# Kernel tuning notes

Hardware: AMD Instinct MI355X
Metric: run time of the kernel (lower is better)

## Reference

```python
import jax, jax.numpy as jnp
import numpy as np

H = 1024

def setup_inputs() -> dict:
    key = jax.random.key(0)
    ks = jax.random.split(key, 7)
    s = 1.0 / np.sqrt(H)
    return {
        "hidden_states": jax.random.normal(ks[0], (4, 2048, H), dtype=jnp.float32),
        "Wq": jax.random.uniform(ks[1], (H, H), jnp.float32, -s, s),
        "bq": jax.random.uniform(ks[2], (H,), jnp.float32, -s, s),
        "Wk": jax.random.uniform(ks[3], (H, H), jnp.float32, -s, s),
        "bk": jax.random.uniform(ks[4], (H,), jnp.float32, -s, s),
        "Wv": jax.random.uniform(ks[5], (H, H), jnp.float32, -s, s),
        "bv": jax.random.uniform(ks[6], (H,), jnp.float32, -s, s),
    }

def reference(hidden_states, Wq, bq, Wk, bk, Wv, bv):
    # Linear projections (torch Linear: x @ W.T + b)
    q = hidden_states @ Wq.T + bq  # [B,S,H]
    k = hidden_states @ Wk.T + bk
    v = hidden_states @ Wv.T + bv
    # Unscaled attention
    probs = jax.nn.softmax(jnp.einsum("bqh,bkh->bqk", q, k), axis=-1)  # [B,S,S]
    attention_scores = jnp.sum(probs, axis=-2)  # [B,S] column sums
    context = jnp.einsum("bqk,bkh->bqh", probs, v)  # [B,S,H]
    return (context, attention_scores)
```

## Files before the change

kernel.cpp:

```cpp
#include <hip/hip_runtime.h>
#include <stdint.h>


typedef __attribute__((ext_vector_type(8))) short short8;
typedef __attribute__((ext_vector_type(4))) float floatx4;
typedef __attribute__((ext_vector_type(4))) unsigned short ushort4v;
typedef unsigned short u16;

__device__ __forceinline__ u16 f2bf(float f) {
  union { float f; uint32_t u; } v; v.f = f;
  uint32_t u = v.u;
  return (u16)((u + 0x7FFFu + ((u >> 16) & 1u)) >> 16);
}
__device__ __forceinline__ float bf2f(u16 h) {
  union { uint32_t u; float f; } v; v.u = ((uint32_t)h) << 16; return v.f;
}

#define AS3(p) ((__attribute__((address_space(3))) void*)(uint32_t)(uintptr_t)(p))
#define AS1(p) ((__attribute__((address_space(1))) void*)(uintptr_t)(p))

__global__ __launch_bounds__(256) void cvt_all_kernel(
    const float* __restrict__ hs, const float* __restrict__ Wq,
    const float* __restrict__ Wk, const float* __restrict__ Wv,
    u16* __restrict__ hsb, u16* __restrict__ Wb, float* __restrict__ lsum) {
  const int bx = blockIdx.x;
  const float* src;
  u16* dst;
  int i;
  if (bx < 8192) {
    i = bx * 1024 + threadIdx.x * 4;
    src = hs; dst = hsb;
  } else {
    const int idx = bx - 8192;
    const int p = idx >> 10, blk = idx & 1023;
    src = (p == 0) ? Wq : (p == 1) ? Wk : Wv;
    dst = Wb + p * 1048576;
    i = blk * 1024 + threadIdx.x * 4;
  }
  const float4 v = *(const float4*)(src + i);
  ushort4v o;
  o[0] = f2bf(v.x); o[1] = f2bf(v.y); o[2] = f2bf(v.z); o[3] = f2bf(v.w);
  *(ushort4v*)(dst + i) = o;
  if (bx == 0) {
    float4 z = {0.f, 0.f, 0.f, 0.f};
#pragma unroll
    for (int k = 0; k < 8; ++k)
      *(float4*)(lsum + threadIdx.x * 32 + k * 4) = z;
  }
}

#define DC_SLOT 24576

template <int NT>
__device__ __forceinline__ void deep_core(const u16* __restrict__ A,
                                          const u16* __restrict__ B,
                                          int lda, int ldb,
                                          u16* smem, floatx4 acc[4][4]) {
  const int tid  = threadIdx.x;
  const int lane = tid & 63;
  const int w    = tid >> 6;
  const int wm   = w >> 1;
  const int wn   = w & 1;
  const int fr   = lane & 15;
  const int quad = lane >> 4;
  const int pc0  = (quad ^ (fr & 7)) * 8;
  const int pc1  = ((4 + quad) ^ (fr & 7)) * 8;

  const u16* pA[4]; uint32_t dA[4];
#pragma unroll
  for (int j = 0; j < 4; ++j) {
    const int c = tid + j * 512, row = c >> 3, kc = c & 7;
    pA[j] = A + row * lda + (kc ^ (row & 7)) * 8;
    dA[j] = c * 8;
  }
  const u16* pB[2]; uint32_t dB[2];
#pragma unroll
  for (int j = 0; j < 2; ++j) {
    const int c = tid + j * 512, row = c >> 3, kc = c & 7;
    pB[j] = B + row * ldb + (kc ^ (row & 7)) * 8;
    dB[j] = 16384 + c * 8;
  }

#define DC_STA(u) do { u16* s_ = smem + ((u) % 3) * DC_SLOT;                                  \
    _Pragma("unroll") for (int j_ = 0; j_ < 4; ++j_)                                           \
      __builtin_amdgcn_global_load_lds(AS1(pA[j_] + (u) * 64), AS3(s_ + dA[j_]), 16, 0, 0);   \
  } while (0)
#define DC_STB(u) do { u16* s_ = smem + ((u) % 3) * DC_SLOT;                                  \
    _Pragma("unroll") for (int j_ = 0; j_ < 2; ++j_)                                           \
      __builtin_amdgcn_global_load_lds(AS1(pB[j_] + (u) * 64), AS3(s_ + dB[j_]), 16, 0, 0);   \
  } while (0)

  DC_STA(0); DC_STB(0); DC_STA(1); DC_STB(1);
  asm volatile("s_waitcnt vmcnt(6)" ::: "memory");
  __builtin_amdgcn_s_barrier();

  const int arow0 = wm * 64 + fr;
  const int brow0 = wn * 64 + fr;

#pragma unroll
  for (int t = 0; t < NT; ++t) {
    const u16* sA = smem + (t % 3) * DC_SLOT;
    const u16* sB = sA + 16384;
    short8 af[4], bf[4];

#pragma unroll
    for (int mi = 0; mi < 4; ++mi)
      af[mi] = *(const short8*)(sA + (arow0 + mi * 16) * 64 + pc0);
#pragma unroll
    for (int ni = 0; ni < 4; ++ni)
      bf[ni] = *(const short8*)(sB + (brow0 + ni * 16) * 64 + pc0);
    if (t < NT - 2) DC_STA(t + 2);
    __builtin_amdgcn_s_barrier();
    asm volatile("s_waitcnt lgkmcnt(0)" ::: "memory");
    __builtin_amdgcn_sched_barrier(0);
    __builtin_amdgcn_s_setprio(1);
#pragma unroll
    for (int mi = 0; mi < 4; ++mi)
#pragma unroll
      for (int ni = 0; ni < 4; ++ni)
        acc[mi][ni] = __builtin_amdgcn_mfma_f32_16x16x32_bf16(af[mi], bf[ni],
                                                              acc[mi][ni], 0, 0, 0);
    __builtin_amdgcn_s_setprio(0);
    __builtin_amdgcn_s_barrier();

#pragma unroll
    for (int mi = 0; mi < 4; ++mi)
      af[mi] = *(const short8*)(sA + (arow0 + mi * 16) * 64 + pc1);
#pragma unroll
    for (int ni = 0; ni < 4; ++ni)
      bf[ni] = *(const short8*)(sB + (brow0 + ni * 16) * 64 + pc1);
    if (t < NT - 2) {
      DC_STB(t + 2);
      asm volatile("s_waitcnt vmcnt(6)" ::: "memory");
    } else {
      asm volatile("s_waitcnt vmcnt(0)" ::: "memory");
    }
    __builtin_amdgcn_s_barrier();
    asm volatile("s_waitcnt lgkmcnt(0)" ::: "memory");
    __builtin_amdgcn_sched_barrier(0);
    __builtin_amdgcn_s_setprio(1);
#pragma unroll
    for (int mi = 0; mi < 4; ++mi)
#pragma unroll
      for (int ni = 0; ni < 4; ++ni)
        acc[mi][ni] = __builtin_amdgcn_mfma_f32_16x16x32_bf16(af[mi], bf[ni],
                                                              acc[mi][ni], 0, 0, 0);
    __builtin_amdgcn_s_setprio(0);
    __builtin_amdgcn_s_barrier();
  }
#undef DC_STA
#undef DC_STB
}

__global__ __launch_bounds__(512, 2) void proj_deep_kernel(
    const u16* __restrict__ hsb, const u16* __restrict__ Wb,
    const float* __restrict__ bq, const float* __restrict__ bk,
    const float* __restrict__ bv,
    u16* __restrict__ qo, u16* __restrict__ ko, u16* __restrict__ vt) {
  extern __shared__ __align__(16) u16 smem[];
  floatx4 acc[4][4];
#pragma unroll
  for (int i = 0; i < 4; ++i)
#pragma unroll
    for (int j = 0; j < 4; ++j) acc[i][j] = {0.f, 0.f, 0.f, 0.f};

  const int p    = blockIdx.z;
  const int flat = blockIdx.x + blockIdx.y * 8;
  const int swz  = (flat & 7) * 32 + (flat >> 3);
  const int m0   = (swz >> 3) * 256;
  const int n0   = (swz & 7) * 128;

  deep_core<16>(hsb + m0 * 1024, Wb + p * 1048576 + n0 * 1024, 1024, 1024, smem, acc);

  const float* bias = (p == 0) ? bq : (p == 1) ? bk : bv;
  const int lane = threadIdx.x & 63, w = threadIdx.x >> 6;
  const int wm = w >> 1, wn = w & 1;
  const int fr = lane & 15, rg4 = (lane >> 4) * 4;

  if (p < 2) {
    u16* out = (p == 0) ? qo : ko;
#pragma unroll
    for (int mi = 0; mi < 4; ++mi)
#pragma unroll
      for (int ni = 0; ni < 4; ++ni) {
        const int n = n0 + wn * 64 + ni * 16 + fr;
        const float bn = bias[n];
#pragma unroll
        for (int r = 0; r < 4; ++r) {
          const int m = m0 + wm * 64 + mi * 16 + rg4 + r;
          out[m * 1024 + n] = f2bf(acc[mi][ni][r] + bn);
        }
      }
  } else {
#pragma unroll
    for (int mi = 0; mi < 4; ++mi) {
      const int mbase = m0 + wm * 64 + mi * 16 + rg4;
      const int b = mbase >> 11, s = mbase & 2047;
#pragma unroll
      for (int ni = 0; ni < 4; ++ni) {
        const int n = n0 + wn * 64 + ni * 16 + fr;
        const float bn = bias[n];
        ushort4v pk;
#pragma unroll
        for (int r = 0; r < 4; ++r) pk[r] = f2bf(acc[mi][ni][r] + bn);
        *(ushort4v*)(vt + b * 2097152 + n * 2048 + s) = pk;
      }
    }
  }
}

__global__ __launch_bounds__(512, 2) void logits_deep_kernel(
    const u16* __restrict__ q, const u16* __restrict__ k,
    u16* __restrict__ E, float* __restrict__ lsum) {
  extern __shared__ __align__(16) u16 smem[];
  floatx4 acc[4][4];
#pragma unroll
  for (int i = 0; i < 4; ++i)
#pragma unroll
    for (int j = 0; j < 4; ++j) acc[i][j] = {0.f, 0.f, 0.f, 0.f};

  const int flat = blockIdx.x + blockIdx.y * 16 + blockIdx.z * 128;
  const int swz  = (flat & 7) * 64 + (flat >> 3);
  const int b    = swz >> 7;
  const int m0   = ((swz >> 4) & 7) * 256;
  const int n0   = (swz & 15) * 128;

  deep_core<16>(q + (b * 2048 + m0) * 1024, k + (b * 2048 + n0) * 1024,
                1024, 1024, smem, acc);

  const int lane = threadIdx.x & 63, w = threadIdx.x >> 6;
  const int wm = w >> 1, wn = w & 1;
  const int fr = lane & 15, quad = lane >> 4;
  u16* Eb = E + b * 4194304;
  float* lb = lsum + b * 2048;

#pragma unroll
  for (int mi = 0; mi < 4; ++mi) {
    floatx4 rs = {0.f, 0.f, 0.f, 0.f};
    const int rbase = m0 + wm * 64 + mi * 16 + quad * 4;
#pragma unroll
    for (int ni = 0; ni < 4; ++ni) {
      const int n = n0 + wn * 64 + ni * 16 + fr;
#pragma unroll
      for (int r = 0; r < 4; ++r) {
        const float e = __expf(acc[mi][ni][r]);
        rs[r] += e;
        Eb[(rbase + r) * 2048 + n] = f2bf(e);
      }
    }
#pragma unroll
    for (int off = 1; off < 16; off <<= 1) {
      rs[0] += __shfl_xor(rs[0], off, 64);
      rs[1] += __shfl_xor(rs[1], off, 64);
      rs[2] += __shfl_xor(rs[2], off, 64);
      rs[3] += __shfl_xor(rs[3], off, 64);
    }
    if (fr == 0) {
#pragma unroll
      for (int r = 0; r < 4; ++r) atomicAdd(&lb[rbase + r], rs[r]);
    }
  }
}

__global__ __launch_bounds__(512, 2) void context_deep_kernel(
    const u16* __restrict__ E, const u16* __restrict__ vt,
    const float* __restrict__ lsum, float* __restrict__ out) {
  extern __shared__ __align__(16) u16 smem[];
  floatx4 acc[4][4];
#pragma unroll
  for (int i = 0; i < 4; ++i)
#pragma unroll
    for (int j = 0; j < 4; ++j) acc[i][j] = {0.f, 0.f, 0.f, 0.f};

  const int flat = blockIdx.x + blockIdx.y * 8 + blockIdx.z * 64;
  const int swz  = (flat & 7) * 32 + (flat >> 3);
  const int b    = swz >> 6;
  const int m0   = ((swz >> 3) & 7) * 256;
  const int n0   = (swz & 7) * 128;

  deep_core<32>(E + b * 4194304 + m0 * 2048, vt + b * 2097152 + n0 * 2048,
                2048, 2048, smem, acc);

  const int lane = threadIdx.x & 63, w = threadIdx.x >> 6;
  const int wm = w >> 1, wn = w & 1;
  const int fr = lane & 15, rg4 = (lane >> 4) * 4;
  const float* lb = lsum + b * 2048;

#pragma unroll
  for (int mi = 0; mi < 4; ++mi) {
    const int rbase = m0 + wm * 64 + mi * 16 + rg4;
    float rinv[4];
#pragma unroll
    for (int r = 0; r < 4; ++r) rinv[r] = 1.0f / lb[rbase + r];
#pragma unroll
    for (int ni = 0; ni < 4; ++ni) {
      const int n = n0 + wn * 64 + ni * 16 + fr;
#pragma unroll
      for (int r = 0; r < 4; ++r)
        out[(b * 2048 + rbase + r) * 1024 + n] = acc[mi][ni][r] * rinv[r];
    }
  }
}

__global__ __launch_bounds__(256) void colsum_part_kernel(
    const u16* __restrict__ E, const float* __restrict__ lsum,
    float* __restrict__ part) {
  const int b  = blockIdx.x;
  const int g  = blockIdx.y;
  const int q0 = g * 64;
  const int j  = threadIdx.x * 8;
  const u16* Eb = E + b * 4194304;
  const float* lb = lsum + b * 2048;
  float acc[8];
#pragma unroll
  for (int c = 0; c < 8; ++c) acc[c] = 0.f;
  for (int r = 0; r < 64; ++r) {
    const int qi = q0 + r;
    const float rinv = 1.0f / lb[qi];
    const short8 ev = *(const short8*)(Eb + qi * 2048 + j);
#pragma unroll
    for (int c = 0; c < 8; ++c) acc[c] += bf2f((u16)ev[c]) * rinv;
  }
  float* pb = part + (b * 32 + g) * 2048 + j;
#pragma unroll
  for (int c = 0; c < 8; ++c) pb[c] = acc[c];
}

__global__ __launch_bounds__(256) void colsum_reduce_kernel(
    const float* __restrict__ part, float* __restrict__ scores) {
  const int b = blockIdx.x;
  const int j = blockIdx.y * 256 + threadIdx.x;
  const float* pb = part + b * 32 * 2048 + j;
  float s = 0.f;
#pragma unroll
  for (int g = 0; g < 32; ++g) s += pb[g * 2048];
  scores[b * 2048 + j] = s;
}

extern "C" void kernel_launch(void* const* d_in, const int* in_sizes, int n_in,
                              void* d_out, int out_size, void* d_ws, size_t ws_size,
                              hipStream_t stream) {
  const float* hs = (const float*)d_in[0];
  const float* Wq = (const float*)d_in[1];
  const float* bq = (const float*)d_in[2];
  const float* Wk = (const float*)d_in[3];
  const float* bk = (const float*)d_in[4];
  const float* Wv = (const float*)d_in[5];
  const float* bv = (const float*)d_in[6];

  char* ws = (char*)d_ws;
  u16*   qw  = (u16*)(ws);
  u16*   kw  = (u16*)(ws + (16u << 20));
  u16*   vtw = (u16*)(ws + (32u << 20));
  float* lw  = (float*)(ws + (48u << 20));
  float* pw  = (float*)(ws + (48u << 20) + (128u << 10));
  u16*   hsb = (u16*)(ws + (49u << 20));
  u16*   Wb  = (u16*)(ws + (65u << 20));
  u16*   Ew  = (u16*)(ws + (49u << 20));

  float* outc = (float*)d_out;
  float* outs = outc + 8388608;

  static int s_attr_done = 0;
  if (!s_attr_done) {
    (void)hipFuncSetAttribute((const void*)proj_deep_kernel,
                              hipFuncAttributeMaxDynamicSharedMemorySize, 147456);
    (void)hipFuncSetAttribute((const void*)logits_deep_kernel,
                              hipFuncAttributeMaxDynamicSharedMemorySize, 147456);
    (void)hipFuncSetAttribute((const void*)context_deep_kernel,
                              hipFuncAttributeMaxDynamicSharedMemorySize, 147456);
    s_attr_done = 1;
  }

  cvt_all_kernel<<<11264, 256, 0, stream>>>(hs, Wq, Wk, Wv, hsb, Wb, lw);
  proj_deep_kernel<<<dim3(8, 32, 3), 512, 147456, stream>>>(hsb, Wb, bq, bk, bv, qw, kw, vtw);
  logits_deep_kernel<<<dim3(16, 8, 4), 512, 147456, stream>>>(qw, kw, Ew, lw);
  context_deep_kernel<<<dim3(8, 8, 4), 512, 147456, stream>>>(Ew, vtw, lw, outc);
  colsum_part_kernel<<<dim3(4, 32), 256, 0, stream>>>(Ew, lw, pw);
  colsum_reduce_kernel<<<dim3(4, 8), 256, 0, stream>>>(pw, outs);
}
```

Before: 241.4 us.

## Use 256x256 logits tiles with quadrant-pipelined MFMA and widen conversion and colsum work

Replaces the 256x128 logits GEMM with a 256x256-tile kernel. It double-buffers LDS and splits each k-step into four quadrant MFMA phases, interleaved with global-to-LDS loads for the next step, which raises operand reuse and halves the block count. The fp32-to-bf16 conversion kernel now handles 8 elements per thread, and the colsum partial kernel gets twice the blocks with 4 columns each for more parallelism. It also adjusts the deep_core tail wait. The risks are higher register pressure and fewer blocks (256) on the large logits GEMM, with possible occupancy or tail effects.

```diff
diff --git a/kernel.cpp b/kernel.cpp
--- a/kernel.cpp
+++ b/kernel.cpp
@@ -5,6 +5,7 @@
 typedef __attribute__((ext_vector_type(8))) short short8;
 typedef __attribute__((ext_vector_type(4))) float floatx4;
 typedef __attribute__((ext_vector_type(4))) unsigned short ushort4v;
+typedef __attribute__((ext_vector_type(8))) unsigned short ushort8v;
 typedef unsigned short u16;
 
 __device__ __forceinline__ u16 f2bf(float f) {
@@ -27,20 +28,22 @@
   const float* src;
   u16* dst;
   int i;
-  if (bx < 8192) {
-    i = bx * 1024 + threadIdx.x * 4;
+  if (bx < 4096) {
+    i = bx * 2048 + threadIdx.x * 8;
     src = hs; dst = hsb;
   } else {
-    const int idx = bx - 8192;
-    const int p = idx >> 10, blk = idx & 1023;
+    const int idx = bx - 4096;
+    const int p = idx >> 9, blk = idx & 511;
     src = (p == 0) ? Wq : (p == 1) ? Wk : Wv;
     dst = Wb + p * 1048576;
-    i = blk * 1024 + threadIdx.x * 4;
-  }
-  const float4 v = *(const float4*)(src + i);
-  ushort4v o;
-  o[0] = f2bf(v.x); o[1] = f2bf(v.y); o[2] = f2bf(v.z); o[3] = f2bf(v.w);
-  *(ushort4v*)(dst + i) = o;
+    i = blk * 2048 + threadIdx.x * 8;
+  }
+  const float4 v0 = *(const float4*)(src + i);
+  const float4 v1 = *(const float4*)(src + i + 4);
+  ushort8v o;
+  o[0] = f2bf(v0.x); o[1] = f2bf(v0.y); o[2] = f2bf(v0.z); o[3] = f2bf(v0.w);
+  o[4] = f2bf(v1.x); o[5] = f2bf(v1.y); o[6] = f2bf(v1.z); o[7] = f2bf(v1.w);
+  *(ushort8v*)(dst + i) = o;
   if (bx == 0) {
     float4 z = {0.f, 0.f, 0.f, 0.f};
 #pragma unroll
@@ -49,7 +52,7 @@
   }
 }
 
-#define DC_SLOT 24576
+#define DC_SLOTU 24576
 
 template <int NT>
 __device__ __forceinline__ void deep_core(const u16* __restrict__ A,
@@ -81,11 +84,11 @@
     dB[j] = 16384 + c * 8;
   }
 
-#define DC_STA(u) do { u16* s_ = smem + ((u) % 3) * DC_SLOT;                                  \
+#define DC_STA(u) do { u16* s_ = smem + ((u) % 3) * DC_SLOTU;                                  \
     _Pragma("unroll") for (int j_ = 0; j_ < 4; ++j_)                                           \
       __builtin_amdgcn_global_load_lds(AS1(pA[j_] + (u) * 64), AS3(s_ + dA[j_]), 16, 0, 0);   \
   } while (0)
-#define DC_STB(u) do { u16* s_ = smem + ((u) % 3) * DC_SLOT;                                  \
+#define DC_STB(u) do { u16* s_ = smem + ((u) % 3) * DC_SLOTU;                                  \
     _Pragma("unroll") for (int j_ = 0; j_ < 2; ++j_)                                           \
       __builtin_amdgcn_global_load_lds(AS1(pB[j_] + (u) * 64), AS3(s_ + dB[j_]), 16, 0, 0);   \
   } while (0)
@@ -99,7 +102,7 @@
 
 #pragma unroll
   for (int t = 0; t < NT; ++t) {
-    const u16* sA = smem + (t % 3) * DC_SLOT;
+    const u16* sA = smem + (t % 3) * DC_SLOTU;
     const u16* sB = sA + 16384;
     short8 af[4], bf[4];
 
@@ -132,7 +135,7 @@
     if (t < NT - 2) {
       DC_STB(t + 2);
       asm volatile("s_waitcnt vmcnt(6)" ::: "memory");
-    } else {
+    } else if (t == NT - 2) {
       asm volatile("s_waitcnt vmcnt(0)" ::: "memory");
     }
     __builtin_amdgcn_s_barrier();
@@ -209,57 +212,157 @@
   }
 }
 
-__global__ __launch_bounds__(512, 2) void logits_deep_kernel(
+__global__ __launch_bounds__(512, 2) void logits_q4_kernel(
     const u16* __restrict__ q, const u16* __restrict__ k,
     u16* __restrict__ E, float* __restrict__ lsum) {
   extern __shared__ __align__(16) u16 smem[];
-  floatx4 acc[4][4];
-#pragma unroll
-  for (int i = 0; i < 4; ++i)
-#pragma unroll
-    for (int j = 0; j < 4; ++j) acc[i][j] = {0.f, 0.f, 0.f, 0.f};
-
-  const int flat = blockIdx.x + blockIdx.y * 16 + blockIdx.z * 128;
-  const int swz  = (flat & 7) * 64 + (flat >> 3);
-  const int b    = swz >> 7;
-  const int m0   = ((swz >> 4) & 7) * 256;
-  const int n0   = (swz & 15) * 128;
-
-  deep_core<16>(q + (b * 2048 + m0) * 1024, k + (b * 2048 + n0) * 1024,
-                1024, 1024, smem, acc);
-
-  const int lane = threadIdx.x & 63, w = threadIdx.x >> 6;
-  const int wm = w >> 1, wn = w & 1;
-  const int fr = lane & 15, quad = lane >> 4;
+  const int tid  = threadIdx.x;
+  const int lane = tid & 63;
+  const int w    = tid >> 6;
+  const int wr4  = w >> 2;
+  const int wc4  = w & 3;
+  const int fr   = lane & 15;
+  const int kq   = lane >> 4;
+  const int pc0  = (kq ^ (fr & 7)) * 8;
+  const int pc1  = ((4 + kq) ^ (fr & 7)) * 8;
+
+  const int flat = blockIdx.x + blockIdx.y * 8 + blockIdx.z * 64;
+  const int swz  = (flat & 7) * 32 + (flat >> 3);
+  const int b    = swz >> 6;
+  const int m0   = ((swz >> 3) & 7) * 256;
+  const int n0   = (swz & 7) * 256;
+
+  const u16* Ag = q + (b * 2048 + m0) * 1024;
+  const u16* Bg = k + (b * 2048 + n0) * 1024;
+
+  const u16* pAs[2]; const u16* pBs[2]; uint32_t dof[2];
+#pragma unroll
+  for (int j = 0; j < 2; ++j) {
+    const int c = tid + j * 512, rl = c >> 3, kc = c & 7;
+    const int gc = (kc ^ (rl & 7)) * 8;
+    pAs[j] = Ag + rl * 1024 + gc;
+    pBs[j] = Bg + rl * 1024 + gc;
+    dof[j] = c * 8;
+  }
+#define ST_A(h, tt, sbase) do { _Pragma("unroll") for (int j_ = 0; j_ < 2; ++j_)      \
+    __builtin_amdgcn_global_load_lds(AS1(pAs[j_] + (h) * 131072 + (tt) * 64),         \
+        AS3(smem + (sbase) + (h) * 8192 + dof[j_]), 16, 0, 0); } while (0)
+#define ST_B(h, tt, sbase) do { _Pragma("unroll") for (int j_ = 0; j_ < 2; ++j_)      \
+    __builtin_amdgcn_global_load_lds(AS1(pBs[j_] + (h) * 131072 + (tt) * 64),         \
+        AS3(smem + (sbase) + 16384 + (h) * 8192 + dof[j_]), 16, 0, 0); } while (0)
+
+  floatx4 acc[2][2][4][2];
+#pragma unroll
+  for (int i = 0; i < 2; ++i)
+#pragma unroll
+    for (int j = 0; j < 2; ++j)
+#pragma unroll
+      for (int mi = 0; mi < 4; ++mi)
+#pragma unroll
+        for (int ni = 0; ni < 2; ++ni) acc[i][j][mi][ni] = {0.f, 0.f, 0.f, 0.f};
+
+  ST_A(0, 0, 0); ST_B(0, 0, 0); ST_B(1, 0, 0); ST_A(1, 0, 0);
+  asm volatile("s_waitcnt vmcnt(4)" ::: "memory");
+  __builtin_amdgcn_s_barrier();
+
+  const int ar0 = wr4 * 64 + fr;
+  const int br0 = wc4 * 32 + fr;
+  short8 af[4][2], bf[2][2];
+
+#define Q4_READ_A(ah) do { _Pragma("unroll") for (int mi = 0; mi < 4; ++mi) {          \
+    af[mi][0] = *(const short8*)(sA + ((ah) * 128 + ar0 + mi * 16) * 64 + pc0);        \
+    af[mi][1] = *(const short8*)(sA + ((ah) * 128 + ar0 + mi * 16) * 64 + pc1); } } while (0)
+#define Q4_READ_B(bh) do { _Pragma("unroll") for (int ni = 0; ni < 2; ++ni) {          \
+    bf[ni][0] = *(const short8*)(sB + ((bh) * 128 + br0 + ni * 16) * 64 + pc0);        \
+    bf[ni][1] = *(const short8*)(sB + ((bh) * 128 + br0 + ni * 16) * 64 + pc1); } } while (0)
+#define Q4_MFMA(ah, bh) do {                                                           \
+    __builtin_amdgcn_s_barrier();                                                      \
+    asm volatile("s_waitcnt lgkmcnt(0)" ::: "memory");                                 \
+    __builtin_amdgcn_sched_barrier(0);                                                 \
+    __builtin_amdgcn_s_setprio(1);                                                     \
+    _Pragma("unroll") for (int mi = 0; mi < 4; ++mi)                                   \
+      _Pragma("unroll") for (int ni = 0; ni < 2; ++ni)                                 \
+        _Pragma("unroll") for (int ks = 0; ks < 2; ++ks)                               \
+          acc[ah][bh][mi][ni] = __builtin_amdgcn_mfma_f32_16x16x32_bf16(               \
+              af[mi][ks], bf[ni][ks], acc[ah][bh][mi][ni], 0, 0, 0);                   \
+    __builtin_amdgcn_s_setprio(0);                                                     \
+    __builtin_amdgcn_s_barrier(); } while (0)
+
+  for (int t = 0; t < 15; ++t) {
+    const uint32_t sb = (uint32_t)(t & 1) * 32768u;
+    const uint32_t sn = (uint32_t)((t + 1) & 1) * 32768u;
+    const u16* sA = smem + sb;
+    const u16* sB = sA + 16384;
+
+    Q4_READ_A(0); Q4_READ_B(0);
+    ST_A(0, t + 1, sn);
+    asm volatile("s_waitcnt vmcnt(4)" ::: "memory");
+    Q4_MFMA(0, 0);
+    Q4_READ_B(1);
+    ST_B(0, t + 1, sn);
+    asm volatile("s_waitcnt vmcnt(4)" ::: "memory");
+    Q4_MFMA(0, 1);
+    Q4_READ_A(1); Q4_READ_B(0);
+    ST_B(1, t + 1, sn);
+    Q4_MFMA(1, 0);
+    Q4_READ_B(1);
+    ST_A(1, t + 1, sn);
+    asm volatile("s_waitcnt vmcnt(4)" ::: "memory");
+    Q4_MFMA(1, 1);
+  }
+
+  {
+    const u16* sA = smem + 32768;
+    const u16* sB = sA + 16384;
+    Q4_READ_A(0); Q4_READ_B(0);
+    asm volatile("s_waitcnt vmcnt(2)" ::: "memory");
+    Q4_MFMA(0, 0);
+    Q4_READ_B(1);
+    asm volatile("s_waitcnt vmcnt(0)" ::: "memory");
+    Q4_MFMA(0, 1);
+    Q4_READ_A(1); Q4_READ_B(0);
+    Q4_MFMA(1, 0);
+    Q4_READ_B(1);
+    Q4_MFMA(1, 1);
+  }
+
   u16* Eb = E + b * 4194304;
   float* lb = lsum + b * 2048;
-
-#pragma unroll
-  for (int mi = 0; mi < 4; ++mi) {
-    floatx4 rs = {0.f, 0.f, 0.f, 0.f};
-    const int rbase = m0 + wm * 64 + mi * 16 + quad * 4;
-#pragma unroll
-    for (int ni = 0; ni < 4; ++ni) {
-      const int n = n0 + wn * 64 + ni * 16 + fr;
-#pragma unroll
-      for (int r = 0; r < 4; ++r) {
-        const float e = __expf(acc[mi][ni][r]);
-        rs[r] += e;
-        Eb[(rbase + r) * 2048 + n] = f2bf(e);
+#pragma unroll
+  for (int ah = 0; ah < 2; ++ah)
+#pragma unroll
+    for (int mi = 0; mi < 4; ++mi) {
+      floatx4 rs = {0.f, 0.f, 0.f, 0.f};
+      const int rbase = m0 + ah * 128 + wr4 * 64 + mi * 16 + kq * 4;
+#pragma unroll
+      for (int bh = 0; bh < 2; ++bh)
+#pragma unroll
+        for (int ni = 0; ni < 2; ++ni) {
+          const int n = n0 + bh * 128 + wc4 * 32 + ni * 16 + fr;
+#pragma unroll
+          for (int r = 0; r < 4; ++r) {
+            const float e = __expf(acc[ah][bh][mi][ni][r]);
+            rs[r] += e;
+            Eb[(rbase + r) * 2048 + n] = f2bf(e);
+          }
+        }
+#pragma unroll
+      for (int off = 1; off < 16; off <<= 1) {
+        rs[0] += __shfl_xor(rs[0], off, 64);
+        rs[1] += __shfl_xor(rs[1], off, 64);
+        rs[2] += __shfl_xor(rs[2], off, 64);
+        rs[3] += __shfl_xor(rs[3], off, 64);
+      }
+      if (fr == 0) {
+#pragma unroll
+        for (int r = 0; r < 4; ++r) atomicAdd(&lb[rbase + r], rs[r]);
       }
     }
-#pragma unroll
-    for (int off = 1; off < 16; off <<= 1) {
-      rs[0] += __shfl_xor(rs[0], off, 64);
-      rs[1] += __shfl_xor(rs[1], off, 64);
-      rs[2] += __shfl_xor(rs[2], off, 64);
-      rs[3] += __shfl_xor(rs[3], off, 64);
-    }
-    if (fr == 0) {
-#pragma unroll
-      for (int r = 0; r < 4; ++r) atomicAdd(&lb[rbase + r], rs[r]);
-    }
-  }
+#undef Q4_READ_A
+#undef Q4_READ_B
+#undef Q4_MFMA
+#undef ST_A
+#undef ST_B
 }
 
 __global__ __launch_bounds__(512, 2) void context_deep_kernel(
@@ -308,22 +411,21 @@
   const int b  = blockIdx.x;
   const int g  = blockIdx.y;
   const int q0 = g * 64;
-  const int j  = threadIdx.x * 8;
+  const int j  = blockIdx.z * 1024 + threadIdx.x * 4;
   const u16* Eb = E + b * 4194304;
   const float* lb = lsum + b * 2048;
-  float acc[8];
-#pragma unroll
-  for (int c = 0; c < 8; ++c) acc[c] = 0.f;
+  float acc[4];
+#pragma unroll
+  for (int c = 0; c < 4; ++c) acc[c] = 0.f;
   for (int r = 0; r < 64; ++r) {
     const int qi = q0 + r;
     const float rinv = 1.0f / lb[qi];
-    const short8 ev = *(const short8*)(Eb + qi * 2048 + j);
-#pragma unroll
-    for (int c = 0; c < 8; ++c) acc[c] += bf2f((u16)ev[c]) * rinv;
-  }
-  float* pb = part + (b * 32 + g) * 2048 + j;
-#pragma unroll
-  for (int c = 0; c < 8; ++c) pb[c] = acc[c];
+    const ushort4v ev = *(const ushort4v*)(Eb + qi * 2048 + j);
+#pragma unroll
+    for (int c = 0; c < 4; ++c) acc[c] += bf2f((u16)ev[c]) * rinv;
+  }
+  float4 o = {acc[0], acc[1], acc[2], acc[3]};
+  *(float4*)(part + (b * 32 + g) * 2048 + j) = o;
 }
 
 __global__ __launch_bounds__(256) void colsum_reduce_kernel(
@@ -365,17 +467,17 @@
   if (!s_attr_done) {
     (void)hipFuncSetAttribute((const void*)proj_deep_kernel,
                               hipFuncAttributeMaxDynamicSharedMemorySize, 147456);
-    (void)hipFuncSetAttribute((const void*)logits_deep_kernel,
-                              hipFuncAttributeMaxDynamicSharedMemorySize, 147456);
+    (void)hipFuncSetAttribute((const void*)logits_q4_kernel,
+                              hipFuncAttributeMaxDynamicSharedMemorySize, 131072);
     (void)hipFuncSetAttribute((const void*)context_deep_kernel,
                               hipFuncAttributeMaxDynamicSharedMemorySize, 147456);
     s_attr_done = 1;
   }
 
-  cvt_all_kernel<<<11264, 256, 0, stream>>>(hs, Wq, Wk, Wv, hsb, Wb, lw);
+  cvt_all_kernel<<<5632, 256, 0, stream>>>(hs, Wq, Wk, Wv, hsb, Wb, lw);
   proj_deep_kernel<<<dim3(8, 32, 3), 512, 147456, stream>>>(hsb, Wb, bq, bk, bv, qw, kw, vtw);
-  logits_deep_kernel<<<dim3(16, 8, 4), 512, 147456, stream>>>(qw, kw, Ew, lw);
+  logits_q4_kernel<<<dim3(8, 8, 4), 512, 131072, stream>>>(qw, kw, Ew, lw);
   context_deep_kernel<<<dim3(8, 8, 4), 512, 147456, stream>>>(Ew, vtw, lw, outc);
-  colsum_part_kernel<<<dim3(4, 32), 256, 0, stream>>>(Ew, lw, pw);
+  colsum_part_kernel<<<dim3(4, 32, 2), 256, 0, stream>>>(Ew, lw, pw);
   colsum_reduce_kernel<<<dim3(4, 8), 256, 0, stream>>>(pw, outs);
 }
```

Result: faster. 235.8 us (-2.3%).
